# Kernel optimization log

Hardware: AMD Instinct MI355X
Metric: run time of the kernel (lower is better)

The kernel has to match this reference:

```python
import jax, jax.numpy as jnp
import numpy as np

N = 100000   # nodes
E = 1600000  # edges (before self-loops)
F_IN = 128
H = 64
G = 512      # graphs in batch


def _add_self_loops(edge_index, n):
    loop = jnp.arange(n, dtype=edge_index.dtype)
    src = jnp.concatenate([edge_index[0], loop])
    dst = jnp.concatenate([edge_index[1], loop])
    return src, dst


def _gcn_norm(src, dst, n):
    # PyG GCNConv: deg over targets with self-loops, norm = d^-1/2[src]*d^-1/2[dst]
    deg = jax.ops.segment_sum(jnp.ones_like(dst, dtype=jnp.float32), dst, num_segments=n)
    dinv = jnp.where(deg > 0, jax.lax.rsqrt(deg), 0.0)
    return dinv[src] * dinv[dst]


def _gcn_conv(x, src, dst, norm, W, b):
    xw = x @ W                                # [N, H]
    msg = xw[src] * norm[:, None]             # [E+N, H] gather + scale
    out = jax.ops.segment_sum(msg, dst, num_segments=x.shape[0])
    return out + b


def setup_inputs() -> dict:
    key = jax.random.key(0)
    ks = jax.random.split(key, 9)
    x = jax.random.normal(ks[0], (N, F_IN), dtype=jnp.float32)
    edge_index = jax.random.randint(ks[1], (2, E), 0, N, dtype=jnp.int32)
    batch = jnp.sort(jax.random.randint(ks[2], (N,), 0, G, dtype=jnp.int32))
    s1 = 1.0 / np.sqrt(F_IN)
    s2 = 1.0 / np.sqrt(H)
    W1 = jax.random.uniform(ks[3], (F_IN, H), jnp.float32, -s1, s1)
    b1 = jnp.zeros((H,), jnp.float32)
    W2 = jax.random.uniform(ks[4], (H, H), jnp.float32, -s2, s2)
    b2 = jnp.zeros((H,), jnp.float32)
    Wl = jax.random.uniform(ks[5], (H, 1), jnp.float32, -s2, s2)
    bl = jnp.zeros((1,), jnp.float32)
    return {"x": x, "edge_index": edge_index, "batch": batch,
            "W1": W1, "b1": b1, "W2": W2, "b2": b2, "Wl": Wl, "bl": bl}


def reference(x, edge_index, batch, W1, b1, W2, b2, Wl, bl):
    n = x.shape[0]
    src, dst = _add_self_loops(edge_index, n)
    norm = _gcn_norm(src, dst, n)
    h = jax.nn.relu(_gcn_conv(x, src, dst, norm, W1, b1))
    h = jax.nn.relu(_gcn_conv(h, src, dst, norm, W2, b2))
    # global mean pool over graphs
    sums = jax.ops.segment_sum(h, batch, num_segments=G)          # [G, H]
    cnt = jax.ops.segment_sum(jnp.ones((n,), jnp.float32), batch, num_segments=G)
    pooled = sums / jnp.maximum(cnt, 1.0)[:, None]
    return jax.nn.sigmoid(pooled @ Wl + bl)                        # [G, 1]
```

## Files before the change

### kernel.cpp

```cpp
#include <hip/hip_runtime.h>
#include <hip/hip_bf16.h>
#include <cmath>

#define F_IN 128
#define HDIM 64
#define NPB 128
#define NB1 512
#define CAP 2560

typedef __attribute__((ext_vector_type(8))) short bf16x8;
typedef __attribute__((ext_vector_type(4))) float f32x4;
typedef __attribute__((ext_vector_type(2))) float f32x2;

__device__ __forceinline__ float bf2f(unsigned short u) {
    union { unsigned int i; float f; } v; v.i = ((unsigned int)u) << 16; return v.f;
}
__device__ __forceinline__ unsigned short f2bf(float f) {
    __hip_bfloat16 h = __float2bfloat16(f);
    union { __hip_bfloat16 h; unsigned short u; } c; c.h = h; return c.u;
}
__device__ __forceinline__ unsigned char f2fp8(float f) {
    int p = __builtin_amdgcn_cvt_pk_fp8_f32(f, f, 0, false);
    return (unsigned char)(p & 0xff);
}
__device__ __forceinline__ void fp8x8_acc(uint2 v, float* a) {
    f32x2 f;
    f = __builtin_amdgcn_cvt_pk_f32_fp8(v.x, false); a[0] += f.x; a[1] += f.y;
    f = __builtin_amdgcn_cvt_pk_f32_fp8(v.x, true);  a[2] += f.x; a[3] += f.y;
    f = __builtin_amdgcn_cvt_pk_f32_fp8(v.y, false); a[4] += f.x; a[5] += f.y;
    f = __builtin_amdgcn_cvt_pk_f32_fp8(v.y, true);  a[6] += f.x; a[7] += f.y;
}


__launch_bounds__(256)
__global__ void p0_count(const int* __restrict__ dst, int* __restrict__ blk_cnt,
                         int E, int nbuk, int chunk,
                         const float* __restrict__ W1, const float* __restrict__ W2,
                         unsigned short* __restrict__ w1t, unsigned short* __restrict__ w2t) {
    int tid = threadIdx.x;
    if (blockIdx.x >= NB1) {
        int t = (blockIdx.x - NB1) * 256 + tid;
        if (t < F_IN * 64) {
            int c = t & 63, k = t >> 6;
            w1t[c * F_IN + k] = f2bf(W1[t]);
        } else if (t < F_IN * 64 + HDIM * 64) {
            int u = t - F_IN * 64;
            int c = u & 63, k = u >> 6;
            w2t[c * HDIM + k] = f2bf(W2[u]);
        }
        return;
    }
    __shared__ int hist[1024];
    for (int i = tid; i < nbuk; i += 256) hist[i] = 0;
    __syncthreads();
    int lo = blockIdx.x * chunk;
    int hi = min(E, lo + chunk);
    for (int e = lo + tid; e < hi; e += 256)
        atomicAdd(&hist[dst[e] >> 7], 1);
    __syncthreads();
    for (int i = tid; i < nbuk; i += 256)
        blk_cnt[i * NB1 + blockIdx.x] = hist[i];
}


__launch_bounds__(256)
__global__ void p_scan_blocks(int* __restrict__ blk_cnt, int* __restrict__ bucket_cnt,
                              int nbuk, const int* __restrict__ batch,
                              int* __restrict__ gstart, int n, int G) {
    int tid = threadIdx.x;
    if (blockIdx.x >= nbuk) {
        int g = (blockIdx.x - nbuk) * 256 + tid;
        if (g > G) return;
        int lo = 0, hi = n;
        while (lo < hi) {
            int mid = (lo + hi) >> 1;
            if (batch[mid] < g) lo = mid + 1; else hi = mid;
        }
        gstart[g] = lo;
        return;
    }
    __shared__ int sd[256];
    int b = blockIdx.x;
    int2* row = (int2*)(blk_cnt + (size_t)b * NB1);
    int2 v = row[tid];
    int s0 = v.x, s1 = s0 + v.y;
    sd[tid] = s1;
    __syncthreads();
    for (int off = 1; off < 256; off <<= 1) {
        int a = (tid >= off) ? sd[tid - off] : 0;
        __syncthreads();
        sd[tid] += a;
        __syncthreads();
    }
    int base = sd[tid] - s1;
    row[tid] = make_int2(base, base + s0);
    if (tid == 255) bucket_cnt[b] = sd[255];
}


__launch_bounds__(256)
__global__ void p1_place(const int* __restrict__ src, const int* __restrict__ dst,
                         const int* __restrict__ blk_cnt, int* __restrict__ pairs,
                         int E, int nbuk, int chunk) {
    __shared__ int cur[1024];
    int tid = threadIdx.x;
    for (int i = tid; i < nbuk; i += 256)
        cur[i] = i * CAP + blk_cnt[i * NB1 + blockIdx.x];
    __syncthreads();
    int lo = blockIdx.x * chunk;
    int hi = min(E, lo + chunk);
    for (int e = lo + tid; e < hi; e += 256) {
        int d = dst[e];
        int pos = atomicAdd(&cur[d >> 7], 1);
        pairs[pos] = (src[e] << 7) | (d & 127);
    }
}


__launch_bounds__(256)
__global__ void p2_csr(const int* __restrict__ pairs, const int* __restrict__ bucket_cnt,
                       float* __restrict__ dinv, int* __restrict__ col,
                       int4* __restrict__ slot_hdr, int n) {
    __shared__ int dl[128];
    __shared__ int sc[128];
    __shared__ int cur[128];
    __shared__ int h64[64];
    __shared__ int s64[64];
    int b = blockIdx.x, tid = threadIdx.x;
    int nlo = b << 7;
    int eb = b * CAP;
    int ee = eb + bucket_cnt[b];
    if (tid < 128) dl[tid] = 0;
    if (tid < 64) h64[tid] = 0;
    __syncthreads();
    for (int e = eb + tid; e < ee; e += 256)
        atomicAdd(&dl[pairs[e] & 127], 1);
    __syncthreads();
    int d0 = 0, excl = 0;
    if (tid < 128) {
        d0 = dl[tid];
        sc[tid] = d0;
    }
    __syncthreads();
    for (int off = 1; off < 128; off <<= 1) {
        int a = (tid >= off && tid < 128) ? sc[tid - off] : 0;
        __syncthreads();
        if (tid < 128) sc[tid] += a;
        __syncthreads();
    }
    if (tid < 128) {
        excl = sc[tid] - d0;
        int node = nlo + tid;
        float dv = rsqrtf((float)(d0 + 1));
        if (node < n) dinv[node] = dv;
        cur[tid] = eb + excl;
        int bin = min(d0, 63);
        atomicAdd(&h64[bin], 1);
    }
    __syncthreads();
    if (tid == 0) { int run = 0; for (int i = 0; i < 64; ++i) { s64[i] = run; run += h64[i]; } }
    __syncthreads();
    if (tid < 64) h64[tid] = 0;
    __syncthreads();
    if (tid < 128) {
        int node = nlo + tid;
        int bin = min(d0, 63);
        int pos = s64[bin] + atomicAdd(&h64[bin], 1);
        float dv = rsqrtf((float)(d0 + 1));
        int4 hdr;
        hdr.x = (node < n) ? node : 0x7fffffff;
        hdr.y = eb + excl;
        hdr.z = d0;
        hdr.w = __float_as_int(dv);
        slot_hdr[nlo + pos] = hdr;
    }
    __syncthreads();
    for (int e = eb + tid; e < ee; e += 256) {
        unsigned int v = (unsigned int)pairs[e];
        int p = atomicAdd(&cur[v & 127], 1);
        col[p] = (int)(v >> 7);
    }
}


template <int K>
__launch_bounds__(256)
__global__ void matmul_mfma(const float* __restrict__ X, const unsigned short* __restrict__ Wt,
                            const float* __restrict__ dinv, unsigned char* __restrict__ out,
                            int n) {
    constexpr int KS  = K / 32;
    constexpr int LDX = K + 8;
    __shared__ unsigned short Xs[64 * LDX];
    __shared__ unsigned short Ws[64 * LDX];

    int tid = threadIdx.x;
    int rowbase = blockIdx.x * 64;

    for (int i = tid; i < 64 * (K / 8); i += 256) {
        int r = i / (K / 8), ch = i % (K / 8);
        *(bf16x8*)(Ws + r * LDX + ch * 8) = ((const bf16x8*)Wt)[i];
    }
    {
        const float4* X4 = (const float4*)X;
        for (int i = tid; i < 64 * (K / 4); i += 256) {
            int r = i / (K / 4), k4 = i % (K / 4);
            ushort4 u = { 0, 0, 0, 0 };
            int gr = rowbase + r;
            if (gr < n) {
                float4 v = X4[(size_t)gr * (K / 4) + k4];
                u.x = f2bf(v.x); u.y = f2bf(v.y); u.z = f2bf(v.z); u.w = f2bf(v.w);
            }
            *(ushort4*)(Xs + r * LDX + k4 * 4) = u;
        }
    }
    __syncthreads();

    int wave = tid >> 6, lane = tid & 63;
    int q = lane >> 4, nn = lane & 15;

    f32x4 acc[4] = {{0,0,0,0},{0,0,0,0},{0,0,0,0},{0,0,0,0}};
    int mrow = wave * 16 + nn;
#pragma unroll
    for (int s = 0; s < KS; ++s) {
        bf16x8 af = *(const bf16x8*)(Xs + mrow * LDX + s * 32 + q * 8);
#pragma unroll
        for (int c = 0; c < 4; ++c) {
            bf16x8 bf = *(const bf16x8*)(Ws + (c * 16 + nn) * LDX + s * 32 + q * 8);
            acc[c] = __builtin_amdgcn_mfma_f32_16x16x32_bf16(af, bf, acc[c], 0, 0, 0);
        }
    }

#pragma unroll
    for (int r = 0; r < 4; ++r) {
        int row = rowbase + wave * 16 + q * 4 + r;
        if (row >= n) continue;
        float dv = dinv[row];
#pragma unroll
        for (int c = 0; c < 4; ++c)
            out[(size_t)row * HDIM + c * 16 + nn] = f2fp8(acc[c][r] * dv);
    }
}


__launch_bounds__(256)
__global__ void matmul_mfma_b16(const unsigned short* __restrict__ X,
                                const unsigned short* __restrict__ Wt,
                                const float* __restrict__ dinv, unsigned char* __restrict__ out,
                                int n) {
    constexpr int K = 64, KS = 2, LDX = K + 8;
    __shared__ unsigned short Xs[64 * LDX];
    __shared__ unsigned short Ws[64 * LDX];

    int tid = threadIdx.x;
    int rowbase = blockIdx.x * 64;

    for (int i = tid; i < 64 * (K / 8); i += 256) {
        int r = i / (K / 8), ch = i % (K / 8);
        *(bf16x8*)(Ws + r * LDX + ch * 8) = ((const bf16x8*)Wt)[i];
    }
    for (int i = tid; i < 64 * 8; i += 256) {
        int r = i >> 3, c = i & 7;
        int gr = rowbase + r;
        bf16x8 u;
        if (gr < n) u = ((const bf16x8*)X)[(size_t)gr * 8 + c];
        else { short z[8] = {0,0,0,0,0,0,0,0}; u = *(bf16x8*)z; }
        *(bf16x8*)(Xs + r * LDX + c * 8) = u;
    }
    __syncthreads();

    int wave = tid >> 6, lane = tid & 63;
    int q = lane >> 4, nn = lane & 15;

    f32x4 acc[4] = {{0,0,0,0},{0,0,0,0},{0,0,0,0},{0,0,0,0}};
    int mrow = wave * 16 + nn;
#pragma unroll
    for (int s = 0; s < KS; ++s) {
        bf16x8 af = *(const bf16x8*)(Xs + mrow * LDX + s * 32 + q * 8);
#pragma unroll
        for (int c = 0; c < 4; ++c) {
            bf16x8 bf = *(const bf16x8*)(Ws + (c * 16 + nn) * LDX + s * 32 + q * 8);
            acc[c] = __builtin_amdgcn_mfma_f32_16x16x32_bf16(af, bf, acc[c], 0, 0, 0);
        }
    }

#pragma unroll
    for (int r = 0; r < 4; ++r) {
        int row = rowbase + wave * 16 + q * 4 + r;
        if (row >= n) continue;
        float dv = dinv[row];
#pragma unroll
        for (int c = 0; c < 4; ++c)
            out[(size_t)row * HDIM + c * 16 + nn] = f2fp8(acc[c][r] * dv);
    }
}


__launch_bounds__(256)
__global__ void csr_gather8_fp8(const int4* __restrict__ slot_hdr, const int* __restrict__ col,
                                const uint2* __restrict__ xws, const float* __restrict__ bias,
                                bf16x8* __restrict__ outb, int nslots, int n) {
    int t = blockIdx.x * 256 + threadIdx.x;
    int slot = t >> 3;
    if (slot >= nslots) return;
    int L = t & 7;
    int4 hdr = slot_hdr[slot];
    int node = hdr.x;
    if (node >= n) return;
    int s = hdr.y;
    int end = s + hdr.z;
    float dv = __int_as_float(hdr.w);

    float a[8] = {0, 0, 0, 0, 0, 0, 0, 0};
    fp8x8_acc(xws[(size_t)node * 8 + L], a);

    int e = s;
    for (; e + 8 <= end; e += 8) {
        uint2 v0 = xws[(size_t)col[e + 0] * 8 + L];
        uint2 v1 = xws[(size_t)col[e + 1] * 8 + L];
        uint2 v2 = xws[(size_t)col[e + 2] * 8 + L];
        uint2 v3 = xws[(size_t)col[e + 3] * 8 + L];
        uint2 v4 = xws[(size_t)col[e + 4] * 8 + L];
        uint2 v5 = xws[(size_t)col[e + 5] * 8 + L];
        uint2 v6 = xws[(size_t)col[e + 6] * 8 + L];
        uint2 v7 = xws[(size_t)col[e + 7] * 8 + L];
        fp8x8_acc(v0, a); fp8x8_acc(v1, a); fp8x8_acc(v2, a); fp8x8_acc(v3, a);
        fp8x8_acc(v4, a); fp8x8_acc(v5, a); fp8x8_acc(v6, a); fp8x8_acc(v7, a);
    }
    for (; e + 4 <= end; e += 4) {
        uint2 v0 = xws[(size_t)col[e + 0] * 8 + L];
        uint2 v1 = xws[(size_t)col[e + 1] * 8 + L];
        uint2 v2 = xws[(size_t)col[e + 2] * 8 + L];
        uint2 v3 = xws[(size_t)col[e + 3] * 8 + L];
        fp8x8_acc(v0, a); fp8x8_acc(v1, a); fp8x8_acc(v2, a); fp8x8_acc(v3, a);
    }
    for (; e < end; ++e)
        fp8x8_acc(xws[(size_t)col[e] * 8 + L], a);

    int f0 = L * 8;
    bf16x8 o;
#pragma unroll
    for (int j = 0; j < 8; ++j)
        o[j] = (short)f2bf(fmaxf(fmaf(a[j], dv, bias[f0 + j]), 0.0f));
    outb[(size_t)node * 8 + L] = o;
}


__launch_bounds__(256)
__global__ void pool_head(const unsigned short* __restrict__ h, const int* __restrict__ gstart,
                          const float* __restrict__ Wl, const float* __restrict__ bl,
                          float* __restrict__ out, int G) {
    int g = blockIdx.x;
    int s = gstart[g], e = gstart[g + 1];
    int f  = threadIdx.x & 63;
    int rg = threadIdx.x >> 6;
    float acc = 0.0f;
    for (int i = s + rg; i < e; i += 4)
        acc += bf2f(h[(size_t)i * HDIM + f]);
    __shared__ float red[4][HDIM];
    red[rg][f] = acc;
    __syncthreads();
    if (rg == 0) {
        float v = (red[0][f] + red[1][f]) + (red[2][f] + red[3][f]);
        float c = fmaxf((float)(e - s), 1.0f);
        v = v * Wl[f] * (1.0f / c);
#pragma unroll
        for (int off = 32; off; off >>= 1) v += __shfl_down(v, off, 64);
        if (f == 0) out[g] = 1.0f / (1.0f + expf(-(v + bl[0])));
    }
}


extern "C" void kernel_launch(void* const* d_in, const int* in_sizes, int n_in,
                              void* d_out, int out_size, void* d_ws, size_t ws_size,
                              hipStream_t stream) {
    const float* x   = (const float*)d_in[0];
    const int* ei    = (const int*)d_in[1];
    const int* batch = (const int*)d_in[2];
    const float* W1  = (const float*)d_in[3];
    const float* b1  = (const float*)d_in[4];
    const float* W2  = (const float*)d_in[5];
    const float* b2  = (const float*)d_in[6];
    const float* Wl  = (const float*)d_in[7];
    const float* bl  = (const float*)d_in[8];
    float* out = (float*)d_out;

    const int n = in_sizes[0] / F_IN;
    const int E = in_sizes[1] / 2;
    const int G = out_size;

    const int* srcp = ei;
    const int* dstp = ei + E;

    int nbuk = (n + NPB - 1) / NPB;
    int nslots = nbuk * NPB;

    char* wsb = (char*)d_ws;
    auto alloc = [&](size_t bytes) { char* p = wsb; wsb += (bytes + 255) & ~(size_t)255; return p; };
    float* dinv       = (float*)alloc((size_t)n * 4);
    int4*  slot_hdr   = (int4*)alloc((size_t)nslots * 16);
    int*   bucket_cnt = (int*)alloc(1024 * 4);
    int*   blk_cnt    = (int*)alloc((size_t)nbuk * NB1 * 4);
    int*   pairs      = (int*)alloc((size_t)nbuk * CAP * 4);
    int*   colx       = (int*)alloc((size_t)nbuk * CAP * 4);
    unsigned short* w1t  = (unsigned short*)alloc((size_t)F_IN * HDIM * 2);
    unsigned short* w2t  = (unsigned short*)alloc((size_t)HDIM * HDIM * 2);
    unsigned char*  xws8 = (unsigned char*)alloc((size_t)n * HDIM);
    unsigned short* xh1  = (unsigned short*)alloc((size_t)n * HDIM * 2);
    unsigned short* xh2  = (unsigned short*)alloc((size_t)n * HDIM * 2);
    int*   gstart     = (int*)alloc(((size_t)G + 1) * 4);

    const int TB = 256;
    int gMM  = (n + 63) / 64;
    int chunk = (E + NB1 - 1) / NB1;
    int gG8  = (nslots * 8 + TB - 1) / TB;

    p0_count<<<NB1 + 48, TB, 0, stream>>>(dstp, blk_cnt, E, nbuk, chunk, W1, W2, w1t, w2t);
    p_scan_blocks<<<nbuk + 3, TB, 0, stream>>>(blk_cnt, bucket_cnt, nbuk, batch, gstart, n, G);
    p1_place<<<NB1, TB, 0, stream>>>(srcp, dstp, blk_cnt, pairs, E, nbuk, chunk);
    p2_csr<<<nbuk, TB, 0, stream>>>(pairs, bucket_cnt, dinv, colx, slot_hdr, n);

    matmul_mfma<F_IN><<<gMM, 256, 0, stream>>>(x, w1t, dinv, xws8, n);
    csr_gather8_fp8<<<gG8, TB, 0, stream>>>(slot_hdr, colx, (const uint2*)xws8,
                                            b1, (bf16x8*)xh1, nslots, n);

    matmul_mfma_b16<<<gMM, 256, 0, stream>>>(xh1, w2t, dinv, xws8, n);
    csr_gather8_fp8<<<gG8, TB, 0, stream>>>(slot_hdr, colx, (const uint2*)xws8,
                                            b2, (bf16x8*)xh2, nslots, n);

    pool_head<<<G, 256, 0, stream>>>(xh2, gstart, Wl, bl, out, G);
}
```

Before: 243.4 us.

## Fuse all pipeline stages into one cooperative persistent kernel with grid syncs

Replaces the nine separate kernel launches (edge counting, scan, placement, CSR build, two matmuls, two gathers, pooling) with a single cooperative kernel whose phases are separated by grid-wide syncs, each phase running grid-stride loops over its work. This removes per-launch overhead and inter-kernel gaps. It also raises the count of virtual edge blocks from 512 to 1024, so the scan uses int4 rows. In exchange, every phase is limited to the occupancy-bounded persistent grid. Each grid.sync adds its own cost, and the kernel now calls the device-property and occupancy queries on every launch.

Result: slower. 809.0 us (+232.3%).

```diff
diff --git a/kernel.cpp b/kernel.cpp
--- a/kernel.cpp
+++ b/kernel.cpp
@@ -1,11 +1,14 @@
 #include <hip/hip_runtime.h>
+#include <hip/hip_cooperative_groups.h>
 #include <hip/hip_bf16.h>
 #include <cmath>
+
+namespace cg = cooperative_groups;
 
 #define F_IN 128
 #define HDIM 64
 #define NPB 128
-#define NB1 512
+#define VNB 1024
 #define CAP 2560
 
 typedef __attribute__((ext_vector_type(8))) short bf16x8;
@@ -31,341 +34,348 @@
     f = __builtin_amdgcn_cvt_pk_f32_fp8(v.y, true);  a[6] += f.x; a[7] += f.y;
 }
 
-
-__launch_bounds__(256)
-__global__ void p0_count(const int* __restrict__ dst, int* __restrict__ blk_cnt,
-                         int E, int nbuk, int chunk,
-                         const float* __restrict__ W1, const float* __restrict__ W2,
-                         unsigned short* __restrict__ w1t, unsigned short* __restrict__ w2t) {
-    int tid = threadIdx.x;
-    if (blockIdx.x >= NB1) {
-        int t = (blockIdx.x - NB1) * 256 + tid;
+struct MegaParams {
+    const float* x; const int* src; const int* dst; const int* batch;
+    const float* W1; const float* b1; const float* W2; const float* b2;
+    const float* Wl; const float* bl; float* out;
+    int n, E, G, nbuk, chunk, ntiles, nslots;
+    int* blk_cnt; int* bucket_cnt; int* pairs; int* colx;
+    unsigned short* w1t; unsigned short* w2t;
+    float* dinv; int4* slot_hdr;
+    unsigned char* xws8; unsigned short* xh1; unsigned short* xh2;
+    int* gstart;
+};
+
+#define SMEM_BYTES 34816
+
+__launch_bounds__(256, 4)
+__global__ void mega_kernel(MegaParams p) {
+    __shared__ __align__(16) char SMEM[SMEM_BYTES];
+    cg::grid_group grid = cg::this_grid();
+    int bid = blockIdx.x, tid = threadIdx.x;
+    int nb = gridDim.x;
+
+    {
+        int* hist = (int*)SMEM;
+        for (int vb = bid; vb < VNB; vb += nb) {
+            for (int i = tid; i < p.nbuk; i += 256) hist[i] = 0;
+            __syncthreads();
+            int lo = vb * p.chunk, hi = min(p.E, lo + p.chunk);
+            for (int e = lo + tid; e < hi; e += 256)
+                atomicAdd(&hist[p.dst[e] >> 7], 1);
+            __syncthreads();
+            for (int i = tid; i < p.nbuk; i += 256)
+                p.blk_cnt[(size_t)i * VNB + vb] = hist[i];
+            __syncthreads();
+        }
+        int t = bid * 256 + tid;
         if (t < F_IN * 64) {
             int c = t & 63, k = t >> 6;
-            w1t[c * F_IN + k] = f2bf(W1[t]);
+            p.w1t[c * F_IN + k] = f2bf(p.W1[t]);
         } else if (t < F_IN * 64 + HDIM * 64) {
             int u = t - F_IN * 64;
             int c = u & 63, k = u >> 6;
-            w2t[c * HDIM + k] = f2bf(W2[u]);
-        }
-        return;
-    }
-    __shared__ int hist[1024];
-    for (int i = tid; i < nbuk; i += 256) hist[i] = 0;
-    __syncthreads();
-    int lo = blockIdx.x * chunk;
-    int hi = min(E, lo + chunk);
-    for (int e = lo + tid; e < hi; e += 256)
-        atomicAdd(&hist[dst[e] >> 7], 1);
-    __syncthreads();
-    for (int i = tid; i < nbuk; i += 256)
-        blk_cnt[i * NB1 + blockIdx.x] = hist[i];
-}
-
-
-__launch_bounds__(256)
-__global__ void p_scan_blocks(int* __restrict__ blk_cnt, int* __restrict__ bucket_cnt,
-                              int nbuk, const int* __restrict__ batch,
-                              int* __restrict__ gstart, int n, int G) {
-    int tid = threadIdx.x;
-    if (blockIdx.x >= nbuk) {
-        int g = (blockIdx.x - nbuk) * 256 + tid;
-        if (g > G) return;
-        int lo = 0, hi = n;
-        while (lo < hi) {
-            int mid = (lo + hi) >> 1;
-            if (batch[mid] < g) lo = mid + 1; else hi = mid;
-        }
-        gstart[g] = lo;
-        return;
-    }
-    __shared__ int sd[256];
-    int b = blockIdx.x;
-    int2* row = (int2*)(blk_cnt + (size_t)b * NB1);
-    int2 v = row[tid];
-    int s0 = v.x, s1 = s0 + v.y;
-    sd[tid] = s1;
-    __syncthreads();
-    for (int off = 1; off < 256; off <<= 1) {
-        int a = (tid >= off) ? sd[tid - off] : 0;
-        __syncthreads();
-        sd[tid] += a;
-        __syncthreads();
-    }
-    int base = sd[tid] - s1;
-    row[tid] = make_int2(base, base + s0);
-    if (tid == 255) bucket_cnt[b] = sd[255];
-}
-
-
-__launch_bounds__(256)
-__global__ void p1_place(const int* __restrict__ src, const int* __restrict__ dst,
-                         const int* __restrict__ blk_cnt, int* __restrict__ pairs,
-                         int E, int nbuk, int chunk) {
-    __shared__ int cur[1024];
-    int tid = threadIdx.x;
-    for (int i = tid; i < nbuk; i += 256)
-        cur[i] = i * CAP + blk_cnt[i * NB1 + blockIdx.x];
-    __syncthreads();
-    int lo = blockIdx.x * chunk;
-    int hi = min(E, lo + chunk);
-    for (int e = lo + tid; e < hi; e += 256) {
-        int d = dst[e];
-        int pos = atomicAdd(&cur[d >> 7], 1);
-        pairs[pos] = (src[e] << 7) | (d & 127);
-    }
-}
-
-
-__launch_bounds__(256)
-__global__ void p2_csr(const int* __restrict__ pairs, const int* __restrict__ bucket_cnt,
-                       float* __restrict__ dinv, int* __restrict__ col,
-                       int4* __restrict__ slot_hdr, int n) {
-    __shared__ int dl[128];
-    __shared__ int sc[128];
-    __shared__ int cur[128];
-    __shared__ int h64[64];
-    __shared__ int s64[64];
-    int b = blockIdx.x, tid = threadIdx.x;
-    int nlo = b << 7;
-    int eb = b * CAP;
-    int ee = eb + bucket_cnt[b];
-    if (tid < 128) dl[tid] = 0;
-    if (tid < 64) h64[tid] = 0;
-    __syncthreads();
-    for (int e = eb + tid; e < ee; e += 256)
-        atomicAdd(&dl[pairs[e] & 127], 1);
-    __syncthreads();
-    int d0 = 0, excl = 0;
-    if (tid < 128) {
-        d0 = dl[tid];
-        sc[tid] = d0;
-    }
-    __syncthreads();
-    for (int off = 1; off < 128; off <<= 1) {
-        int a = (tid >= off && tid < 128) ? sc[tid - off] : 0;
-        __syncthreads();
-        if (tid < 128) sc[tid] += a;
-        __syncthreads();
-    }
-    if (tid < 128) {
-        excl = sc[tid] - d0;
-        int node = nlo + tid;
-        float dv = rsqrtf((float)(d0 + 1));
-        if (node < n) dinv[node] = dv;
-        cur[tid] = eb + excl;
-        int bin = min(d0, 63);
-        atomicAdd(&h64[bin], 1);
-    }
-    __syncthreads();
-    if (tid == 0) { int run = 0; for (int i = 0; i < 64; ++i) { s64[i] = run; run += h64[i]; } }
-    __syncthreads();
-    if (tid < 64) h64[tid] = 0;
-    __syncthreads();
-    if (tid < 128) {
-        int node = nlo + tid;
-        int bin = min(d0, 63);
-        int pos = s64[bin] + atomicAdd(&h64[bin], 1);
-        float dv = rsqrtf((float)(d0 + 1));
-        int4 hdr;
-        hdr.x = (node < n) ? node : 0x7fffffff;
-        hdr.y = eb + excl;
-        hdr.z = d0;
-        hdr.w = __float_as_int(dv);
-        slot_hdr[nlo + pos] = hdr;
-    }
-    __syncthreads();
-    for (int e = eb + tid; e < ee; e += 256) {
-        unsigned int v = (unsigned int)pairs[e];
-        int p = atomicAdd(&cur[v & 127], 1);
-        col[p] = (int)(v >> 7);
-    }
-}
-
-
-template <int K>
-__launch_bounds__(256)
-__global__ void matmul_mfma(const float* __restrict__ X, const unsigned short* __restrict__ Wt,
-                            const float* __restrict__ dinv, unsigned char* __restrict__ out,
-                            int n) {
-    constexpr int KS  = K / 32;
-    constexpr int LDX = K + 8;
-    __shared__ unsigned short Xs[64 * LDX];
-    __shared__ unsigned short Ws[64 * LDX];
-
-    int tid = threadIdx.x;
-    int rowbase = blockIdx.x * 64;
-
-    for (int i = tid; i < 64 * (K / 8); i += 256) {
-        int r = i / (K / 8), ch = i % (K / 8);
-        *(bf16x8*)(Ws + r * LDX + ch * 8) = ((const bf16x8*)Wt)[i];
-    }
-    {
-        const float4* X4 = (const float4*)X;
-        for (int i = tid; i < 64 * (K / 4); i += 256) {
-            int r = i / (K / 4), k4 = i % (K / 4);
-            ushort4 u = { 0, 0, 0, 0 };
-            int gr = rowbase + r;
-            if (gr < n) {
-                float4 v = X4[(size_t)gr * (K / 4) + k4];
-                u.x = f2bf(v.x); u.y = f2bf(v.y); u.z = f2bf(v.z); u.w = f2bf(v.w);
-            }
-            *(ushort4*)(Xs + r * LDX + k4 * 4) = u;
-        }
-    }
-    __syncthreads();
-
-    int wave = tid >> 6, lane = tid & 63;
-    int q = lane >> 4, nn = lane & 15;
-
-    f32x4 acc[4] = {{0,0,0,0},{0,0,0,0},{0,0,0,0},{0,0,0,0}};
-    int mrow = wave * 16 + nn;
-#pragma unroll
-    for (int s = 0; s < KS; ++s) {
-        bf16x8 af = *(const bf16x8*)(Xs + mrow * LDX + s * 32 + q * 8);
-#pragma unroll
-        for (int c = 0; c < 4; ++c) {
-            bf16x8 bf = *(const bf16x8*)(Ws + (c * 16 + nn) * LDX + s * 32 + q * 8);
-            acc[c] = __builtin_amdgcn_mfma_f32_16x16x32_bf16(af, bf, acc[c], 0, 0, 0);
-        }
-    }
-
-#pragma unroll
-    for (int r = 0; r < 4; ++r) {
-        int row = rowbase + wave * 16 + q * 4 + r;
-        if (row >= n) continue;
-        float dv = dinv[row];
-#pragma unroll
-        for (int c = 0; c < 4; ++c)
-            out[(size_t)row * HDIM + c * 16 + nn] = f2fp8(acc[c][r] * dv);
-    }
-}
-
-
-__launch_bounds__(256)
-__global__ void matmul_mfma_b16(const unsigned short* __restrict__ X,
-                                const unsigned short* __restrict__ Wt,
-                                const float* __restrict__ dinv, unsigned char* __restrict__ out,
-                                int n) {
-    constexpr int K = 64, KS = 2, LDX = K + 8;
-    __shared__ unsigned short Xs[64 * LDX];
-    __shared__ unsigned short Ws[64 * LDX];
-
-    int tid = threadIdx.x;
-    int rowbase = blockIdx.x * 64;
-
-    for (int i = tid; i < 64 * (K / 8); i += 256) {
-        int r = i / (K / 8), ch = i % (K / 8);
-        *(bf16x8*)(Ws + r * LDX + ch * 8) = ((const bf16x8*)Wt)[i];
-    }
-    for (int i = tid; i < 64 * 8; i += 256) {
-        int r = i >> 3, c = i & 7;
-        int gr = rowbase + r;
-        bf16x8 u;
-        if (gr < n) u = ((const bf16x8*)X)[(size_t)gr * 8 + c];
-        else { short z[8] = {0,0,0,0,0,0,0,0}; u = *(bf16x8*)z; }
-        *(bf16x8*)(Xs + r * LDX + c * 8) = u;
-    }
-    __syncthreads();
-
-    int wave = tid >> 6, lane = tid & 63;
-    int q = lane >> 4, nn = lane & 15;
-
-    f32x4 acc[4] = {{0,0,0,0},{0,0,0,0},{0,0,0,0},{0,0,0,0}};
-    int mrow = wave * 16 + nn;
-#pragma unroll
-    for (int s = 0; s < KS; ++s) {
-        bf16x8 af = *(const bf16x8*)(Xs + mrow * LDX + s * 32 + q * 8);
-#pragma unroll
-        for (int c = 0; c < 4; ++c) {
-            bf16x8 bf = *(const bf16x8*)(Ws + (c * 16 + nn) * LDX + s * 32 + q * 8);
-            acc[c] = __builtin_amdgcn_mfma_f32_16x16x32_bf16(af, bf, acc[c], 0, 0, 0);
-        }
-    }
-
-#pragma unroll
-    for (int r = 0; r < 4; ++r) {
-        int row = rowbase + wave * 16 + q * 4 + r;
-        if (row >= n) continue;
-        float dv = dinv[row];
-#pragma unroll
-        for (int c = 0; c < 4; ++c)
-            out[(size_t)row * HDIM + c * 16 + nn] = f2fp8(acc[c][r] * dv);
-    }
-}
-
-
-__launch_bounds__(256)
-__global__ void csr_gather8_fp8(const int4* __restrict__ slot_hdr, const int* __restrict__ col,
-                                const uint2* __restrict__ xws, const float* __restrict__ bias,
-                                bf16x8* __restrict__ outb, int nslots, int n) {
-    int t = blockIdx.x * 256 + threadIdx.x;
-    int slot = t >> 3;
-    if (slot >= nslots) return;
-    int L = t & 7;
-    int4 hdr = slot_hdr[slot];
-    int node = hdr.x;
-    if (node >= n) return;
-    int s = hdr.y;
-    int end = s + hdr.z;
-    float dv = __int_as_float(hdr.w);
-
-    float a[8] = {0, 0, 0, 0, 0, 0, 0, 0};
-    fp8x8_acc(xws[(size_t)node * 8 + L], a);
-
-    int e = s;
-    for (; e + 8 <= end; e += 8) {
-        uint2 v0 = xws[(size_t)col[e + 0] * 8 + L];
-        uint2 v1 = xws[(size_t)col[e + 1] * 8 + L];
-        uint2 v2 = xws[(size_t)col[e + 2] * 8 + L];
-        uint2 v3 = xws[(size_t)col[e + 3] * 8 + L];
-        uint2 v4 = xws[(size_t)col[e + 4] * 8 + L];
-        uint2 v5 = xws[(size_t)col[e + 5] * 8 + L];
-        uint2 v6 = xws[(size_t)col[e + 6] * 8 + L];
-        uint2 v7 = xws[(size_t)col[e + 7] * 8 + L];
-        fp8x8_acc(v0, a); fp8x8_acc(v1, a); fp8x8_acc(v2, a); fp8x8_acc(v3, a);
-        fp8x8_acc(v4, a); fp8x8_acc(v5, a); fp8x8_acc(v6, a); fp8x8_acc(v7, a);
-    }
-    for (; e + 4 <= end; e += 4) {
-        uint2 v0 = xws[(size_t)col[e + 0] * 8 + L];
-        uint2 v1 = xws[(size_t)col[e + 1] * 8 + L];
-        uint2 v2 = xws[(size_t)col[e + 2] * 8 + L];
-        uint2 v3 = xws[(size_t)col[e + 3] * 8 + L];
-        fp8x8_acc(v0, a); fp8x8_acc(v1, a); fp8x8_acc(v2, a); fp8x8_acc(v3, a);
-    }
-    for (; e < end; ++e)
-        fp8x8_acc(xws[(size_t)col[e] * 8 + L], a);
-
-    int f0 = L * 8;
-    bf16x8 o;
-#pragma unroll
-    for (int j = 0; j < 8; ++j)
-        o[j] = (short)f2bf(fmaxf(fmaf(a[j], dv, bias[f0 + j]), 0.0f));
-    outb[(size_t)node * 8 + L] = o;
-}
-
-
-__launch_bounds__(256)
-__global__ void pool_head(const unsigned short* __restrict__ h, const int* __restrict__ gstart,
-                          const float* __restrict__ Wl, const float* __restrict__ bl,
-                          float* __restrict__ out, int G) {
-    int g = blockIdx.x;
-    int s = gstart[g], e = gstart[g + 1];
-    int f  = threadIdx.x & 63;
-    int rg = threadIdx.x >> 6;
-    float acc = 0.0f;
-    for (int i = s + rg; i < e; i += 4)
-        acc += bf2f(h[(size_t)i * HDIM + f]);
-    __shared__ float red[4][HDIM];
-    red[rg][f] = acc;
-    __syncthreads();
-    if (rg == 0) {
-        float v = (red[0][f] + red[1][f]) + (red[2][f] + red[3][f]);
-        float c = fmaxf((float)(e - s), 1.0f);
-        v = v * Wl[f] * (1.0f / c);
-#pragma unroll
-        for (int off = 32; off; off >>= 1) v += __shfl_down(v, off, 64);
-        if (f == 0) out[g] = 1.0f / (1.0f + expf(-(v + bl[0])));
+            p.w2t[c * HDIM + k] = f2bf(p.W2[u]);
+        }
+    }
+    grid.sync();
+
+    {
+        int* sd = (int*)SMEM;
+        for (int b = bid; b < p.nbuk; b += nb) {
+            int4* row = (int4*)(p.blk_cnt + (size_t)b * VNB);
+            int4 v = row[tid];
+            int s0 = v.x, s1 = s0 + v.y, s2 = s1 + v.z, s3 = s2 + v.w;
+            sd[tid] = s3;
+            __syncthreads();
+            for (int off = 1; off < 256; off <<= 1) {
+                int a = (tid >= off) ? sd[tid - off] : 0;
+                __syncthreads();
+                sd[tid] += a;
+                __syncthreads();
+            }
+            int base = sd[tid] - s3;
+            int4 o; o.x = base; o.y = base + s0; o.z = base + s1; o.w = base + s2;
+            row[tid] = o;
+            if (tid == 255) p.bucket_cnt[b] = sd[255];
+            __syncthreads();
+        }
+        int g = bid * 256 + tid;
+        if (g <= p.G) {
+            int lo = 0, hi = p.n;
+            while (lo < hi) {
+                int mid = (lo + hi) >> 1;
+                if (p.batch[mid] < g) lo = mid + 1; else hi = mid;
+            }
+            p.gstart[g] = lo;
+        }
+    }
+    grid.sync();
+
+    {
+        int* cur = (int*)SMEM;
+        for (int vb = bid; vb < VNB; vb += nb) {
+            for (int i = tid; i < p.nbuk; i += 256)
+                cur[i] = i * CAP + p.blk_cnt[(size_t)i * VNB + vb];
+            __syncthreads();
+            int lo = vb * p.chunk, hi = min(p.E, lo + p.chunk);
+            for (int e = lo + tid; e < hi; e += 256) {
+                int d = p.dst[e];
+                int pos = atomicAdd(&cur[d >> 7], 1);
+                p.pairs[pos] = (p.src[e] << 7) | (d & 127);
+            }
+            __syncthreads();
+        }
+    }
+    grid.sync();
+
+    {
+        int* dl  = (int*)SMEM;
+        int* sc  = dl + 128;
+        int* cu  = sc + 128;
+        int* h64 = cu + 128;
+        int* s64 = h64 + 64;
+        for (int b = bid; b < p.nbuk; b += nb) {
+            int nlo = b << 7;
+            int eb = b * CAP;
+            int ee = eb + p.bucket_cnt[b];
+            if (tid < 128) dl[tid] = 0;
+            if (tid < 64) h64[tid] = 0;
+            __syncthreads();
+            for (int e = eb + tid; e < ee; e += 256)
+                atomicAdd(&dl[p.pairs[e] & 127], 1);
+            __syncthreads();
+            int d0 = 0, excl = 0;
+            if (tid < 128) { d0 = dl[tid]; sc[tid] = d0; }
+            __syncthreads();
+            for (int off = 1; off < 128; off <<= 1) {
+                int a = (tid >= off && tid < 128) ? sc[tid - off] : 0;
+                __syncthreads();
+                if (tid < 128) sc[tid] += a;
+                __syncthreads();
+            }
+            if (tid < 128) {
+                excl = sc[tid] - d0;
+                int node = nlo + tid;
+                float dv = rsqrtf((float)(d0 + 1));
+                if (node < p.n) p.dinv[node] = dv;
+                cu[tid] = eb + excl;
+                atomicAdd(&h64[min(d0, 63)], 1);
+            }
+            __syncthreads();
+            if (tid == 0) { int run = 0; for (int i = 0; i < 64; ++i) { s64[i] = run; run += h64[i]; } }
+            __syncthreads();
+            if (tid < 64) h64[tid] = 0;
+            __syncthreads();
+            if (tid < 128) {
+                int node = nlo + tid;
+                int bin = min(d0, 63);
+                int pos = s64[bin] + atomicAdd(&h64[bin], 1);
+                int4 hdr;
+                hdr.x = (node < p.n) ? node : 0x7fffffff;
+                hdr.y = eb + excl;
+                hdr.z = d0;
+                hdr.w = __float_as_int(rsqrtf((float)(d0 + 1)));
+                p.slot_hdr[nlo + pos] = hdr;
+            }
+            __syncthreads();
+            for (int e = eb + tid; e < ee; e += 256) {
+                unsigned int v = (unsigned int)p.pairs[e];
+                int pos = atomicAdd(&cu[v & 127], 1);
+                p.colx[pos] = (int)(v >> 7);
+            }
+            __syncthreads();
+        }
+    }
+    grid.sync();
+
+    {
+        constexpr int K = F_IN, KS = K / 32, LDX = K + 8;
+        unsigned short* Xs = (unsigned short*)SMEM;
+        unsigned short* Ws = (unsigned short*)(SMEM + 64 * LDX * 2);
+        int wave = tid >> 6, lane = tid & 63;
+        int q = lane >> 4, nn = lane & 15;
+        for (int tile = bid; tile < p.ntiles; tile += nb) {
+            int rowbase = tile * 64;
+            for (int i = tid; i < 64 * (K / 8); i += 256) {
+                int r = i / (K / 8), ch = i % (K / 8);
+                *(bf16x8*)(Ws + r * LDX + ch * 8) = ((const bf16x8*)p.w1t)[i];
+            }
+            const float4* X4 = (const float4*)p.x;
+            for (int i = tid; i < 64 * (K / 4); i += 256) {
+                int r = i / (K / 4), k4 = i % (K / 4);
+                ushort4 u = { 0, 0, 0, 0 };
+                int gr = rowbase + r;
+                if (gr < p.n) {
+                    float4 v = X4[(size_t)gr * (K / 4) + k4];
+                    u.x = f2bf(v.x); u.y = f2bf(v.y); u.z = f2bf(v.z); u.w = f2bf(v.w);
+                }
+                *(ushort4*)(Xs + r * LDX + k4 * 4) = u;
+            }
+            __syncthreads();
+            f32x4 acc[4] = {{0,0,0,0},{0,0,0,0},{0,0,0,0},{0,0,0,0}};
+            int mrow = wave * 16 + nn;
+#pragma unroll
+            for (int s = 0; s < KS; ++s) {
+                bf16x8 af = *(const bf16x8*)(Xs + mrow * LDX + s * 32 + q * 8);
+#pragma unroll
+                for (int c = 0; c < 4; ++c) {
+                    bf16x8 bf = *(const bf16x8*)(Ws + (c * 16 + nn) * LDX + s * 32 + q * 8);
+                    acc[c] = __builtin_amdgcn_mfma_f32_16x16x32_bf16(af, bf, acc[c], 0, 0, 0);
+                }
+            }
+#pragma unroll
+            for (int r = 0; r < 4; ++r) {
+                int row = rowbase + wave * 16 + q * 4 + r;
+                if (row >= p.n) continue;
+                float dv = p.dinv[row];
+#pragma unroll
+                for (int c = 0; c < 4; ++c)
+                    p.xws8[(size_t)row * HDIM + c * 16 + nn] = f2fp8(acc[c][r] * dv);
+            }
+            __syncthreads();
+        }
+    }
+    grid.sync();
+
+    {
+        const uint2* xws = (const uint2*)p.xws8;
+        for (int t = bid * 256 + tid; t < p.nslots * 8; t += nb * 256) {
+            int slot = t >> 3, L = t & 7;
+            int4 hdr = p.slot_hdr[slot];
+            int node = hdr.x;
+            if (node >= p.n) continue;
+            int s = hdr.y, end = s + hdr.z;
+            float dv = __int_as_float(hdr.w);
+            float a[8] = {0, 0, 0, 0, 0, 0, 0, 0};
+            fp8x8_acc(xws[(size_t)node * 8 + L], a);
+            int e = s;
+            for (; e + 8 <= end; e += 8) {
+                uint2 v0 = xws[(size_t)p.colx[e + 0] * 8 + L];
+                uint2 v1 = xws[(size_t)p.colx[e + 1] * 8 + L];
+                uint2 v2 = xws[(size_t)p.colx[e + 2] * 8 + L];
+                uint2 v3 = xws[(size_t)p.colx[e + 3] * 8 + L];
+                uint2 v4 = xws[(size_t)p.colx[e + 4] * 8 + L];
+                uint2 v5 = xws[(size_t)p.colx[e + 5] * 8 + L];
+                uint2 v6 = xws[(size_t)p.colx[e + 6] * 8 + L];
+                uint2 v7 = xws[(size_t)p.colx[e + 7] * 8 + L];
+                fp8x8_acc(v0, a); fp8x8_acc(v1, a); fp8x8_acc(v2, a); fp8x8_acc(v3, a);
+                fp8x8_acc(v4, a); fp8x8_acc(v5, a); fp8x8_acc(v6, a); fp8x8_acc(v7, a);
+            }
+            for (; e < end; ++e)
+                fp8x8_acc(xws[(size_t)p.colx[e] * 8 + L], a);
+            int f0 = L * 8;
+            bf16x8 o;
+#pragma unroll
+            for (int j = 0; j < 8; ++j)
+                o[j] = (short)f2bf(fmaxf(fmaf(a[j], dv, p.b1[f0 + j]), 0.0f));
+            ((bf16x8*)p.xh1)[(size_t)node * 8 + L] = o;
+        }
+    }
+    grid.sync();
+
+    {
+        constexpr int K = HDIM, KS = K / 32, LDX = K + 8;
+        unsigned short* Xs = (unsigned short*)SMEM;
+        unsigned short* Ws = (unsigned short*)(SMEM + 64 * LDX * 2);
+        int wave = tid >> 6, lane = tid & 63;
+        int q = lane >> 4, nn = lane & 15;
+        for (int tile = bid; tile < p.ntiles; tile += nb) {
+            int rowbase = tile * 64;
+            for (int i = tid; i < 64 * (K / 8); i += 256) {
+                int r = i / (K / 8), ch = i % (K / 8);
+                *(bf16x8*)(Ws + r * LDX + ch * 8) = ((const bf16x8*)p.w2t)[i];
+            }
+            for (int i = tid; i < 64 * 8; i += 256) {
+                int r = i >> 3, c = i & 7;
+                int gr = rowbase + r;
+                bf16x8 u;
+                if (gr < p.n) u = ((const bf16x8*)p.xh1)[(size_t)gr * 8 + c];
+                else { short z[8] = {0,0,0,0,0,0,0,0}; u = *(bf16x8*)z; }
+                *(bf16x8*)(Xs + r * LDX + c * 8) = u;
+            }
+            __syncthreads();
+            f32x4 acc[4] = {{0,0,0,0},{0,0,0,0},{0,0,0,0},{0,0,0,0}};
+            int mrow = wave * 16 + nn;
+#pragma unroll
+            for (int s = 0; s < KS; ++s) {
+                bf16x8 af = *(const bf16x8*)(Xs + mrow * LDX + s * 32 + q * 8);
+#pragma unroll
+                for (int c = 0; c < 4; ++c) {
+                    bf16x8 bf = *(const bf16x8*)(Ws + (c * 16 + nn) * LDX + s * 32 + q * 8);
+                    acc[c] = __builtin_amdgcn_mfma_f32_16x16x32_bf16(af, bf, acc[c], 0, 0, 0);
+                }
+            }
+#pragma unroll
+            for (int r = 0; r < 4; ++r) {
+                int row = rowbase + wave * 16 + q * 4 + r;
+                if (row >= p.n) continue;
+                float dv = p.dinv[row];
+#pragma unroll
+                for (int c = 0; c < 4; ++c)
+                    p.xws8[(size_t)row * HDIM + c * 16 + nn] = f2fp8(acc[c][r] * dv);
+            }
+            __syncthreads();
+        }
+    }
+    grid.sync();
+
+    {
+        const uint2* xws = (const uint2*)p.xws8;
+        for (int t = bid * 256 + tid; t < p.nslots * 8; t += nb * 256) {
+            int slot = t >> 3, L = t & 7;
+            int4 hdr = p.slot_hdr[slot];
+            int node = hdr.x;
+            if (node >= p.n) continue;
+            int s = hdr.y, end = s + hdr.z;
+            float dv = __int_as_float(hdr.w);
+            float a[8] = {0, 0, 0, 0, 0, 0, 0, 0};
+            fp8x8_acc(xws[(size_t)node * 8 + L], a);
+            int e = s;
+            for (; e + 8 <= end; e += 8) {
+                uint2 v0 = xws[(size_t)p.colx[e + 0] * 8 + L];
+                uint2 v1 = xws[(size_t)p.colx[e + 1] * 8 + L];
+                uint2 v2 = xws[(size_t)p.colx[e + 2] * 8 + L];
+                uint2 v3 = xws[(size_t)p.colx[e + 3] * 8 + L];
+                uint2 v4 = xws[(size_t)p.colx[e + 4] * 8 + L];
+                uint2 v5 = xws[(size_t)p.colx[e + 5] * 8 + L];
+                uint2 v6 = xws[(size_t)p.colx[e + 6] * 8 + L];
+                uint2 v7 = xws[(size_t)p.colx[e + 7] * 8 + L];
+                fp8x8_acc(v0, a); fp8x8_acc(v1, a); fp8x8_acc(v2, a); fp8x8_acc(v3, a);
+                fp8x8_acc(v4, a); fp8x8_acc(v5, a); fp8x8_acc(v6, a); fp8x8_acc(v7, a);
+            }
+            for (; e < end; ++e)
+                fp8x8_acc(xws[(size_t)p.colx[e] * 8 + L], a);
+            int f0 = L * 8;
+            bf16x8 o;
+#pragma unroll
+            for (int j = 0; j < 8; ++j)
+                o[j] = (short)f2bf(fmaxf(fmaf(a[j], dv, p.b2[f0 + j]), 0.0f));
+            ((bf16x8*)p.xh2)[(size_t)node * 8 + L] = o;
+        }
+    }
+    grid.sync();
+
+    {
+        float (*red)[HDIM] = (float(*)[HDIM])SMEM;
+        int f = tid & 63, rg = tid >> 6;
+        for (int g = bid; g < p.G; g += nb) {
+            int s = p.gstart[g], e = p.gstart[g + 1];
+            float acc = 0.0f;
+            for (int i = s + rg; i < e; i += 4)
+                acc += bf2f(p.xh2[(size_t)i * HDIM + f]);
+            red[rg][f] = acc;
+            __syncthreads();
+            if (rg == 0) {
+                float v = (red[0][f] + red[1][f]) + (red[2][f] + red[3][f]);
+                float c = fmaxf((float)(e - s), 1.0f);
+                v = v * p.Wl[f] * (1.0f / c);
+#pragma unroll
+                for (int off = 32; off; off >>= 1) v += __shfl_down(v, off, 64);
+                if (f == 0) p.out[g] = 1.0f / (1.0f + expf(-(v + p.bl[0])));
+            }
+            __syncthreads();
+        }
     }
 }
 
@@ -373,59 +383,52 @@
 extern "C" void kernel_launch(void* const* d_in, const int* in_sizes, int n_in,
                               void* d_out, int out_size, void* d_ws, size_t ws_size,
                               hipStream_t stream) {
-    const float* x   = (const float*)d_in[0];
-    const int* ei    = (const int*)d_in[1];
-    const int* batch = (const int*)d_in[2];
-    const float* W1  = (const float*)d_in[3];
-    const float* b1  = (const float*)d_in[4];
-    const float* W2  = (const float*)d_in[5];
-    const float* b2  = (const float*)d_in[6];
-    const float* Wl  = (const float*)d_in[7];
-    const float* bl  = (const float*)d_in[8];
-    float* out = (float*)d_out;
-
     const int n = in_sizes[0] / F_IN;
     const int E = in_sizes[1] / 2;
     const int G = out_size;
-
-    const int* srcp = ei;
-    const int* dstp = ei + E;
-
     int nbuk = (n + NPB - 1) / NPB;
-    int nslots = nbuk * NPB;
 
     char* wsb = (char*)d_ws;
     auto alloc = [&](size_t bytes) { char* p = wsb; wsb += (bytes + 255) & ~(size_t)255; return p; };
-    float* dinv       = (float*)alloc((size_t)n * 4);
-    int4*  slot_hdr   = (int4*)alloc((size_t)nslots * 16);
-    int*   bucket_cnt = (int*)alloc(1024 * 4);
-    int*   blk_cnt    = (int*)alloc((size_t)nbuk * NB1 * 4);
-    int*   pairs      = (int*)alloc((size_t)nbuk * CAP * 4);
-    int*   colx       = (int*)alloc((size_t)nbuk * CAP * 4);
-    unsigned short* w1t  = (unsigned short*)alloc((size_t)F_IN * HDIM * 2);
-    unsigned short* w2t  = (unsigned short*)alloc((size_t)HDIM * HDIM * 2);
-    unsigned char*  xws8 = (unsigned char*)alloc((size_t)n * HDIM);
-    unsigned short* xh1  = (unsigned short*)alloc((size_t)n * HDIM * 2);
-    unsigned short* xh2  = (unsigned short*)alloc((size_t)n * HDIM * 2);
-    int*   gstart     = (int*)alloc(((size_t)G + 1) * 4);
-
-    const int TB = 256;
-    int gMM  = (n + 63) / 64;
-    int chunk = (E + NB1 - 1) / NB1;
-    int gG8  = (nslots * 8 + TB - 1) / TB;
-
-    p0_count<<<NB1 + 48, TB, 0, stream>>>(dstp, blk_cnt, E, nbuk, chunk, W1, W2, w1t, w2t);
-    p_scan_blocks<<<nbuk + 3, TB, 0, stream>>>(blk_cnt, bucket_cnt, nbuk, batch, gstart, n, G);
-    p1_place<<<NB1, TB, 0, stream>>>(srcp, dstp, blk_cnt, pairs, E, nbuk, chunk);
-    p2_csr<<<nbuk, TB, 0, stream>>>(pairs, bucket_cnt, dinv, colx, slot_hdr, n);
-
-    matmul_mfma<F_IN><<<gMM, 256, 0, stream>>>(x, w1t, dinv, xws8, n);
-    csr_gather8_fp8<<<gG8, TB, 0, stream>>>(slot_hdr, colx, (const uint2*)xws8,
-                                            b1, (bf16x8*)xh1, nslots, n);
-
-    matmul_mfma_b16<<<gMM, 256, 0, stream>>>(xh1, w2t, dinv, xws8, n);
-    csr_gather8_fp8<<<gG8, TB, 0, stream>>>(slot_hdr, colx, (const uint2*)xws8,
-                                            b2, (bf16x8*)xh2, nslots, n);
-
-    pool_head<<<G, 256, 0, stream>>>(xh2, gstart, Wl, bl, out, G);
-}
+    MegaParams p;
+    p.x = (const float*)d_in[0];
+    p.src = (const int*)d_in[1];
+    p.dst = p.src + E;
+    p.batch = (const int*)d_in[2];
+    p.W1 = (const float*)d_in[3];
+    p.b1 = (const float*)d_in[4];
+    p.W2 = (const float*)d_in[5];
+    p.b2 = (const float*)d_in[6];
+    p.Wl = (const float*)d_in[7];
+    p.bl = (const float*)d_in[8];
+    p.out = (float*)d_out;
+    p.n = n; p.E = E; p.G = G; p.nbuk = nbuk;
+    p.chunk = (E + VNB - 1) / VNB;
+    p.ntiles = (n + 63) / 64;
+    p.nslots = nbuk * NPB;
+
+    p.dinv       = (float*)alloc((size_t)n * 4);
+    p.slot_hdr   = (int4*)alloc((size_t)p.nslots * 16);
+    p.bucket_cnt = (int*)alloc(1024 * 4);
+    p.blk_cnt    = (int*)alloc((size_t)nbuk * VNB * 4);
+    p.pairs      = (int*)alloc((size_t)nbuk * CAP * 4);
+    p.colx       = (int*)alloc((size_t)nbuk * CAP * 4);
+    p.w1t        = (unsigned short*)alloc((size_t)F_IN * HDIM * 2);
+    p.w2t        = (unsigned short*)alloc((size_t)HDIM * HDIM * 2);
+    p.xws8       = (unsigned char*)alloc((size_t)n * HDIM);
+    p.xh1        = (unsigned short*)alloc((size_t)n * HDIM * 2);
+    p.xh2        = (unsigned short*)alloc((size_t)n * HDIM * 2);
+    p.gstart     = (int*)alloc(((size_t)G + 1) * 4);
+
+    int maxb = 0;
+    hipOccupancyMaxActiveBlocksPerMultiprocessor(&maxb, (const void*)mega_kernel, 256, 0);
+    if (maxb < 1) maxb = 1;
+    hipDeviceProp_t prop;
+    hipGetDeviceProperties(&prop, 0);
+    int grid = maxb * prop.multiProcessorCount;
+    if (grid > 1024) grid = 1024;
+
+    void* args[] = { (void*)&p };
+    hipLaunchCooperativeKernel((const void*)mega_kernel, dim3(grid), dim3(256),
+                               args, 0, stream);
+}
```
